# Kernel tuning notes

Measured on AMD Instinct MI355X. Metric: run time of the kernel, lower is better.

## Reference

```python
import jax, jax.numpy as jnp
import numpy as np

H = 1024
L = 4096


def _gru_cell(x, h, Wih, Whh, bih, bhh):
    # x: [H], h: [H]; PyTorch GRU gate math (gate order: r, z, n)
    gi = Wih @ x + bih            # [3H]
    gh = Whh @ h + bhh            # [3H]
    i_r, i_z, i_n = jnp.split(gi, 3)
    h_r, h_z, h_n = jnp.split(gh, 3)
    r = jax.nn.sigmoid(i_r + h_r)
    z = jax.nn.sigmoid(i_z + h_z)
    n = jnp.tanh(i_n + r * h_n)
    return (1.0 - z) * n + z * h


def _run_gru(xs, Wih, Whh, bih, bhh):
    # xs: [L, H] -> (outputs [L, H], final hidden [H])
    def step(h, x):
        h_new = _gru_cell(x, h, Wih, Whh, bih, bhh)
        return h_new, h_new
    h0 = jnp.zeros((H,), dtype=xs.dtype)
    h_last, outs = jax.lax.scan(step, h0, xs)
    return outs, h_last


def setup_inputs() -> dict:
    key = jax.random.key(0)
    ks = jax.random.split(key, 9)
    s = 1.0 / np.sqrt(H)
    def u(k, shape):
        return jax.random.uniform(k, shape, jnp.float32, -s, s)
    return {
        "x": jax.random.normal(ks[0], (L, H), jnp.float32),
        "fwd_Wih": u(ks[1], (3 * H, H)),
        "fwd_Whh": u(ks[2], (3 * H, H)),
        "fwd_bih": u(ks[3], (3 * H,)),
        "fwd_bhh": u(ks[4], (3 * H,)),
        "rev_Wih": u(ks[5], (3 * H, H)),
        "rev_Whh": u(ks[6], (3 * H, H)),
        "rev_bih": u(ks[7], (3 * H,)),
        "rev_bhh": u(ks[8], (3 * H,)),
    }


def reference(x, fwd_Wih, fwd_Whh, fwd_bih, fwd_bhh,
              rev_Wih, rev_Whh, rev_bih, rev_bhh):
    # Forward direction over x[0..L-1]
    fwd_outs, fwd_h = _run_gru(x, fwd_Wih, fwd_Whh, fwd_bih, fwd_bhh)
    # Reverse direction: iterate from last timestep to first, write back reversed
    rev_outs_r, rev_h = _run_gru(x[::-1], rev_Wih, rev_Whh, rev_bih, rev_bhh)
    rev_outs = rev_outs_r[::-1]
    outputs = jnp.concatenate([fwd_outs, rev_outs], axis=1)     # [L, 2H]
    hidden = jnp.concatenate([fwd_h, rev_h])[None, None, :]     # [1, 1, 2H]
    projected_output = hidden
    return outputs, hidden, projected_output
```

## Files before the change

### kernel.cpp

```cpp
#include <hip/hip_runtime.h>
#include <cstdint>
#include <cstddef>

#define L_SEQ 4096
#define HDIM  1024
#define G3    3072
#define NWG   128
#define SCAN_THREADS 256

#define BM 128
#define BN 128
#define BK 16
#define LPAD 4

__global__ __launch_bounds__(256) void gi_gemm(
    const float* __restrict__ X,
    const float* __restrict__ Wf, const float* __restrict__ bf,
    const float* __restrict__ Wr, const float* __restrict__ br,
    float* __restrict__ GIf, float* __restrict__ GIr)
{
    const int dir = blockIdx.z;
    const float* W  = dir ? Wr : Wf;
    const float* bi = dir ? br : bf;
    float* GI = dir ? GIr : GIf;

    __shared__ float As[BK][BM + LPAD];
    __shared__ float Bs[BK][BN + LPAD];

    const int t  = threadIdx.x;
    const int s0 = blockIdx.x * BM;
    const int r0 = blockIdx.y * BN;

    const int tr = t >> 4;
    const int tc = t & 15;

    float acc[8][8];
#pragma unroll
    for (int i = 0; i < 8; ++i)
#pragma unroll
        for (int j = 0; j < 8; ++j) acc[i][j] = 0.f;

    const int lrow = t >> 2;
    const int lcol = (t & 3) * 4;

    for (int k0 = 0; k0 < HDIM; k0 += BK) {
#pragma unroll
        for (int p = 0; p < 2; ++p) {
            const int row = lrow + 64 * p;
            float4 av = *reinterpret_cast<const float4*>(&X[(size_t)(s0 + row) * HDIM + k0 + lcol]);
            float4 bv = *reinterpret_cast<const float4*>(&W[(size_t)(r0 + row) * HDIM + k0 + lcol]);
            As[lcol + 0][row] = av.x; As[lcol + 1][row] = av.y;
            As[lcol + 2][row] = av.z; As[lcol + 3][row] = av.w;
            Bs[lcol + 0][row] = bv.x; Bs[lcol + 1][row] = bv.y;
            Bs[lcol + 2][row] = bv.z; Bs[lcol + 3][row] = bv.w;
        }
        __syncthreads();
#pragma unroll
        for (int kk = 0; kk < BK; ++kk) {
            float4 a0 = *reinterpret_cast<const float4*>(&As[kk][8 * tr]);
            float4 a1 = *reinterpret_cast<const float4*>(&As[kk][8 * tr + 4]);
            float4 b0 = *reinterpret_cast<const float4*>(&Bs[kk][8 * tc]);
            float4 b1 = *reinterpret_cast<const float4*>(&Bs[kk][8 * tc + 4]);
            float a[8] = {a0.x, a0.y, a0.z, a0.w, a1.x, a1.y, a1.z, a1.w};
            float b[8] = {b0.x, b0.y, b0.z, b0.w, b1.x, b1.y, b1.z, b1.w};
#pragma unroll
            for (int i = 0; i < 8; ++i)
#pragma unroll
                for (int j = 0; j < 8; ++j)
                    acc[i][j] = fmaf(a[i], b[j], acc[i][j]);
        }
        __syncthreads();
    }

#pragma unroll
    for (int i = 0; i < 8; ++i) {
        const int row = s0 + 8 * tr + i;
#pragma unroll
        for (int j = 0; j < 8; ++j) acc[i][j] += bi[r0 + 8 * tc + j];
        float4* dst = reinterpret_cast<float4*>(&GI[(size_t)row * G3 + r0 + 8 * tc]);
        dst[0] = make_float4(acc[i][0], acc[i][1], acc[i][2], acc[i][3]);
        dst[1] = make_float4(acc[i][4], acc[i][5], acc[i][6], acc[i][7]);
    }
}

__global__ __launch_bounds__(SCAN_THREADS, 1) void gru_scan(
    const float* __restrict__ WhhF, const float* __restrict__ WhhR,
    const float* __restrict__ bhhF, const float* __restrict__ bhhR,
    const float* __restrict__ GIf,  const float* __restrict__ GIr,
    float* __restrict__ out,
    unsigned long long* __restrict__ pkF, unsigned long long* __restrict__ pkR)
{
    const int wg  = blockIdx.x;
    const int dir = wg >> 7;
    const int wid = wg & (NWG - 1);
    const float* Whh = dir ? WhhR : WhhF;
    const float* bhh = dir ? bhhR : bhhF;
    const float* GI  = dir ? GIr  : GIf;
    unsigned long long* pk = dir ? pkR : pkF;

    const int t     = threadIdx.x;
    const int wv    = t >> 6;
    const int r_idx = t >> 5;
    const int kp    = t & 31;
    const int j     = wid * 8 + r_idx;

    float wr[32], wz[32], wn[32];
    {
        const float* pr = Whh + (size_t)j * HDIM + kp;
        const float* pz = pr + (size_t)HDIM * HDIM;
        const float* pn = pz + (size_t)HDIM * HDIM;
#pragma unroll
        for (int i = 0; i < 32; ++i) {
            wr[i] = pr[32 * i];
            wz[i] = pz[32 * i];
            wn[i] = pn[32 * i];
        }
    }
#pragma unroll
    for (int i = 0; i < 32; ++i) {
        asm volatile("" : "+v"(wr[i]), "+v"(wz[i]), "+v"(wn[i]));
    }
    const float b_r = bhh[j];
    const float b_z = bhh[HDIM + j];
    const float b_n = bhh[2 * HDIM + j];

    __shared__ float h_lds[2][HDIM];
    __shared__ int   wflag[2][4];
    __shared__ int   rdone[2][4];

    if (t < 8)       wflag[t >> 2][t & 3] = 0;
    else if (t < 16) rdone[(t - 8) >> 2][(t - 8) & 3] = 0;
    __syncthreads();

    float gr = 0.f, gz = 0.f, gn = 0.f;
    if (kp == 0) {
        const float* g = GI + (size_t)(dir ? (L_SEQ - 1) : 0) * G3 + j;
        gr = g[0];
        gz = g[HDIM];
        gn = g[2 * HDIM];
    }

    for (int s = 0; s < L_SEQ; ++s) {
        const int srow = dir ? (L_SEQ - 1 - s) : s;
        const int par  = s & 1;
        const int want = s + 1;

        if (s >= 2) {
            for (;;) {
                int d0 = __hip_atomic_load(&rdone[par][0], __ATOMIC_RELAXED, __HIP_MEMORY_SCOPE_WORKGROUP);
                int d1 = __hip_atomic_load(&rdone[par][1], __ATOMIC_RELAXED, __HIP_MEMORY_SCOPE_WORKGROUP);
                int d2 = __hip_atomic_load(&rdone[par][2], __ATOMIC_RELAXED, __HIP_MEMORY_SCOPE_WORKGROUP);
                int d3 = __hip_atomic_load(&rdone[par][3], __ATOMIC_RELAXED, __HIP_MEMORY_SCOPE_WORKGROUP);
                if (d0 >= s - 1 && d1 >= s - 1 && d2 >= s - 1 && d3 >= s - 1) break;
            }
            __threadfence_block();
        }

        const unsigned long long* src = pk + (size_t)par * HDIM + 4 * t;
        const unsigned wtag = (unsigned)s;
        unsigned long long p0, p1, p2, p3;
        for (;;) {
            p0 = __hip_atomic_load(src + 0, __ATOMIC_RELAXED, __HIP_MEMORY_SCOPE_AGENT);
            p1 = __hip_atomic_load(src + 1, __ATOMIC_RELAXED, __HIP_MEMORY_SCOPE_AGENT);
            p2 = __hip_atomic_load(src + 2, __ATOMIC_RELAXED, __HIP_MEMORY_SCOPE_AGENT);
            p3 = __hip_atomic_load(src + 3, __ATOMIC_RELAXED, __HIP_MEMORY_SCOPE_AGENT);
            if ((unsigned)(p0 >> 32) == wtag && (unsigned)(p1 >> 32) == wtag &&
                (unsigned)(p2 >> 32) == wtag && (unsigned)(p3 >> 32) == wtag)
                break;
        }
        reinterpret_cast<float4*>(h_lds[par])[t] =
            make_float4(__uint_as_float((unsigned)p0), __uint_as_float((unsigned)p1),
                        __uint_as_float((unsigned)p2), __uint_as_float((unsigned)p3));
        __threadfence_block();
        if ((t & 63) == 0)
            __hip_atomic_store(&wflag[par][wv], want, __ATOMIC_RELAXED, __HIP_MEMORY_SCOPE_WORKGROUP);

        float gnr = 0.f, gnz = 0.f, gnn = 0.f;
        if (s + 1 < L_SEQ && kp == 0) {
            const int nrow = dir ? (L_SEQ - 2 - s) : (s + 1);
            const float* g = GI + (size_t)nrow * G3 + j;
            gnr = g[0];
            gnz = g[HDIM];
            gnn = g[2 * HDIM];
        }

        float ar = 0.f, az = 0.f, an = 0.f;
#pragma unroll
        for (int c = 0; c < 4; ++c) {
            for (;;) {
                int f = __hip_atomic_load(&wflag[par][c], __ATOMIC_RELAXED, __HIP_MEMORY_SCOPE_WORKGROUP);
                if (f >= want) break;
            }
            __threadfence_block();
#pragma unroll
            for (int i = 8 * c; i < 8 * c + 8; ++i) {
                const float h = h_lds[par][kp + 32 * i];
                ar = fmaf(wr[i], h, ar);
                az = fmaf(wz[i], h, az);
                an = fmaf(wn[i], h, an);
            }
        }
        const float hold = h_lds[par][j];
        __threadfence_block();
        if ((t & 63) == 0)
            __hip_atomic_store(&rdone[par][wv], want, __ATOMIC_RELAXED, __HIP_MEMORY_SCOPE_WORKGROUP);

#pragma unroll
        for (int off = 16; off > 0; off >>= 1) {
            ar += __shfl_down(ar, off, 32);
            az += __shfl_down(az, off, 32);
            an += __shfl_down(an, off, 32);
        }

        if (kp == 0) {
            const float rr = 1.f / (1.f + __expf(-(gr + ar + b_r)));
            const float zz = 1.f / (1.f + __expf(-(gz + az + b_z)));
            const float xx = gn + rr * (an + b_n);
            const float e  = __expf(-2.f * fabsf(xx));
            float th = (1.f - e) / (1.f + e);
            th = copysignf(th, xx);
            const float hn = (1.f - zz) * th + zz * hold;

            const unsigned long long pkt =
                ((unsigned long long)(unsigned)(s + 1) << 32) | __float_as_uint(hn);
            __hip_atomic_store(pk + (size_t)((s + 1) & 1) * HDIM + j, pkt,
                               __ATOMIC_RELAXED, __HIP_MEMORY_SCOPE_AGENT);

            out[(size_t)srow * (2 * HDIM) + dir * HDIM + j] = hn;
            if (s == L_SEQ - 1) {
                out[(size_t)L_SEQ * 2 * HDIM + dir * HDIM + j] = hn;
                out[(size_t)L_SEQ * 2 * HDIM + 2 * HDIM + dir * HDIM + j] = hn;
            }
        }

        gr = gnr; gz = gnz; gn = gnn;
    }
}

extern "C" void kernel_launch(void* const* d_in, const int* in_sizes, int n_in,
                              void* d_out, int out_size, void* d_ws, size_t ws_size,
                              hipStream_t stream)
{
    (void)in_sizes; (void)n_in; (void)out_size; (void)ws_size;

    const float* x    = (const float*)d_in[0];
    const float* fWih = (const float*)d_in[1];
    const float* fWhh = (const float*)d_in[2];
    const float* fbih = (const float*)d_in[3];
    const float* fbhh = (const float*)d_in[4];
    const float* rWih = (const float*)d_in[5];
    const float* rWhh = (const float*)d_in[6];
    const float* rbih = (const float*)d_in[7];
    const float* rbhh = (const float*)d_in[8];
    float* out = (float*)d_out;

    unsigned long long* pkF = (unsigned long long*)d_ws;
    unsigned long long* pkR = pkF + 2 * HDIM;
    float* GIf = (float*)((char*)d_ws + 32768);
    float* GIr = GIf + (size_t)L_SEQ * G3;

    hipMemsetAsync(d_ws, 0, 32768, stream);

    dim3 gg(L_SEQ / BM, G3 / BN, 2);
    gi_gemm<<<gg, 256, 0, stream>>>(x, fWih, fbih, rWih, rbih, GIf, GIr);

    const float* a0 = fWhh; const float* a1 = rWhh;
    const float* a2 = fbhh; const float* a3 = rbhh;
    const float* a4 = GIf;  const float* a5 = GIr;
    float* a6 = out;
    unsigned long long* a7 = pkF; unsigned long long* a8 = pkR;
    void* args[] = {(void*)&a0, (void*)&a1, (void*)&a2, (void*)&a3,
                    (void*)&a4, (void*)&a5, (void*)&a6, (void*)&a7, (void*)&a8};

    hipError_t err = hipLaunchCooperativeKernel((const void*)gru_scan,
                                                dim3(2 * NWG), dim3(SCAN_THREADS),
                                                args, 0, stream);
    if (err != hipSuccess) {
        gru_scan<<<dim3(2 * NWG), dim3(SCAN_THREADS), 0, stream>>>(
            fWhh, rWhh, fbhh, rbhh, GIf, GIr, out, pkF, pkR);
    }
}
```

Baseline: 8.858 ms.

## Double scan workgroup to 512 threads with one wave per hidden row

The recurrent scan kernel now uses 512 threads per workgroup, so each of the 8 waves owns one hidden row and each lane holds 16 weights per gate instead of 32. The per-step h broadcast uses 2 packed loads per thread instead of 4, and the LDS flag arrays grow to 8 waves. The reduction becomes a 64-wide shuffle. The aim is shorter per-thread dependent FMA chains and polling work on the latency-bound step, at the cost of more waves to synchronize and one extra shuffle level.

```diff
diff --git a/kernel.cpp b/kernel.cpp
--- a/kernel.cpp
+++ b/kernel.cpp
@@ -6,7 +6,7 @@
 #define HDIM  1024
 #define G3    3072
 #define NWG   128
-#define SCAN_THREADS 256
+#define SCAN_THREADS 512
 
 #define BM 128
 #define BN 128
@@ -98,26 +98,25 @@
     const float* GI  = dir ? GIr  : GIf;
     unsigned long long* pk = dir ? pkR : pkF;
 
-    const int t     = threadIdx.x;
-    const int wv    = t >> 6;
-    const int r_idx = t >> 5;
-    const int kp    = t & 31;
-    const int j     = wid * 8 + r_idx;
-
-    float wr[32], wz[32], wn[32];
+    const int t  = threadIdx.x;
+    const int wv = t >> 6;
+    const int kp = t & 63;
+    const int j  = wid * 8 + wv;
+
+    float wr[16], wz[16], wn[16];
     {
         const float* pr = Whh + (size_t)j * HDIM + kp;
         const float* pz = pr + (size_t)HDIM * HDIM;
         const float* pn = pz + (size_t)HDIM * HDIM;
 #pragma unroll
-        for (int i = 0; i < 32; ++i) {
-            wr[i] = pr[32 * i];
-            wz[i] = pz[32 * i];
-            wn[i] = pn[32 * i];
-        }
-    }
-#pragma unroll
-    for (int i = 0; i < 32; ++i) {
+        for (int i = 0; i < 16; ++i) {
+            wr[i] = pr[64 * i];
+            wz[i] = pz[64 * i];
+            wn[i] = pn[64 * i];
+        }
+    }
+#pragma unroll
+    for (int i = 0; i < 16; ++i) {
         asm volatile("" : "+v"(wr[i]), "+v"(wz[i]), "+v"(wn[i]));
     }
     const float b_r = bhh[j];
@@ -125,11 +124,11 @@
     const float b_n = bhh[2 * HDIM + j];
 
     __shared__ float h_lds[2][HDIM];
-    __shared__ int   wflag[2][4];
-    __shared__ int   rdone[2][4];
-
-    if (t < 8)       wflag[t >> 2][t & 3] = 0;
-    else if (t < 16) rdone[(t - 8) >> 2][(t - 8) & 3] = 0;
+    __shared__ int   wflag[2][8];
+    __shared__ int   rdone[2][8];
+
+    if (t < 16)      wflag[t >> 3][t & 7] = 0;
+    else if (t < 32) rdone[(t - 16) >> 3][(t - 16) & 7] = 0;
     __syncthreads();
 
     float gr = 0.f, gz = 0.f, gn = 0.f;
@@ -147,32 +146,29 @@
 
         if (s >= 2) {
             for (;;) {
-                int d0 = __hip_atomic_load(&rdone[par][0], __ATOMIC_RELAXED, __HIP_MEMORY_SCOPE_WORKGROUP);
-                int d1 = __hip_atomic_load(&rdone[par][1], __ATOMIC_RELAXED, __HIP_MEMORY_SCOPE_WORKGROUP);
-                int d2 = __hip_atomic_load(&rdone[par][2], __ATOMIC_RELAXED, __HIP_MEMORY_SCOPE_WORKGROUP);
-                int d3 = __hip_atomic_load(&rdone[par][3], __ATOMIC_RELAXED, __HIP_MEMORY_SCOPE_WORKGROUP);
-                if (d0 >= s - 1 && d1 >= s - 1 && d2 >= s - 1 && d3 >= s - 1) break;
+                int ok = 1;
+#pragma unroll
+                for (int w = 0; w < 8; ++w)
+                    ok &= (__hip_atomic_load(&rdone[par][w], __ATOMIC_RELAXED,
+                                             __HIP_MEMORY_SCOPE_WORKGROUP) >= s - 1);
+                if (ok) break;
             }
             __threadfence_block();
         }
 
-        const unsigned long long* src = pk + (size_t)par * HDIM + 4 * t;
+        const unsigned long long* src = pk + (size_t)par * HDIM + 2 * t;
         const unsigned wtag = (unsigned)s;
-        unsigned long long p0, p1, p2, p3;
+        unsigned long long p0, p1;
         for (;;) {
             p0 = __hip_atomic_load(src + 0, __ATOMIC_RELAXED, __HIP_MEMORY_SCOPE_AGENT);
             p1 = __hip_atomic_load(src + 1, __ATOMIC_RELAXED, __HIP_MEMORY_SCOPE_AGENT);
-            p2 = __hip_atomic_load(src + 2, __ATOMIC_RELAXED, __HIP_MEMORY_SCOPE_AGENT);
-            p3 = __hip_atomic_load(src + 3, __ATOMIC_RELAXED, __HIP_MEMORY_SCOPE_AGENT);
-            if ((unsigned)(p0 >> 32) == wtag && (unsigned)(p1 >> 32) == wtag &&
-                (unsigned)(p2 >> 32) == wtag && (unsigned)(p3 >> 32) == wtag)
+            if ((unsigned)(p0 >> 32) == wtag && (unsigned)(p1 >> 32) == wtag)
                 break;
         }
-        reinterpret_cast<float4*>(h_lds[par])[t] =
-            make_float4(__uint_as_float((unsigned)p0), __uint_as_float((unsigned)p1),
-                        __uint_as_float((unsigned)p2), __uint_as_float((unsigned)p3));
+        reinterpret_cast<float2*>(h_lds[par])[t] =
+            make_float2(__uint_as_float((unsigned)p0), __uint_as_float((unsigned)p1));
         __threadfence_block();
-        if ((t & 63) == 0)
+        if (kp == 0)
             __hip_atomic_store(&wflag[par][wv], want, __ATOMIC_RELAXED, __HIP_MEMORY_SCOPE_WORKGROUP);
 
         float gnr = 0.f, gnz = 0.f, gnn = 0.f;
@@ -186,15 +182,15 @@
 
         float ar = 0.f, az = 0.f, an = 0.f;
 #pragma unroll
-        for (int c = 0; c < 4; ++c) {
+        for (int c = 0; c < 8; ++c) {
             for (;;) {
                 int f = __hip_atomic_load(&wflag[par][c], __ATOMIC_RELAXED, __HIP_MEMORY_SCOPE_WORKGROUP);
                 if (f >= want) break;
             }
             __threadfence_block();
 #pragma unroll
-            for (int i = 8 * c; i < 8 * c + 8; ++i) {
-                const float h = h_lds[par][kp + 32 * i];
+            for (int i = 2 * c; i < 2 * c + 2; ++i) {
+                const float h = h_lds[par][kp + 64 * i];
                 ar = fmaf(wr[i], h, ar);
                 az = fmaf(wz[i], h, az);
                 an = fmaf(wn[i], h, an);
@@ -202,14 +198,14 @@
         }
         const float hold = h_lds[par][j];
         __threadfence_block();
-        if ((t & 63) == 0)
+        if (kp == 0)
             __hip_atomic_store(&rdone[par][wv], want, __ATOMIC_RELAXED, __HIP_MEMORY_SCOPE_WORKGROUP);
 
 #pragma unroll
-        for (int off = 16; off > 0; off >>= 1) {
-            ar += __shfl_down(ar, off, 32);
-            az += __shfl_down(az, off, 32);
-            an += __shfl_down(an, off, 32);
+        for (int off = 32; off > 0; off >>= 1) {
+            ar += __shfl_down(ar, off, 64);
+            az += __shfl_down(az, off, 64);
+            an += __shfl_down(an, off, 64);
         }
 
         if (kp == 0) {
```

After: 10.61 ms. 19.8% more time.
